# Performance work log

Measured on AMD Instinct MI355X. Metric: run time of the kernel, lower is better.

## Reference

```python
import jax, jax.numpy as jnp
import numpy as np

KERNEL_SIZE = 7  # must be odd
PAD = KERNEL_SIZE // 2


def setup_inputs() -> dict:
    key = jax.random.key(0)
    k1, k2 = jax.random.split(key)
    B, C, H, W = 8, 128, 256, 256
    x = jax.random.normal(k1, (B, C, H, W), dtype=jnp.float32)
    y = jax.random.normal(k2, (B, C, H, W), dtype=jnp.float32)
    return {"x": x, "y": y}


def reference(x, y):
    # x, y: [B, C, H, W] -> coef: [B, K*K, H, W]
    B, C, H, W = x.shape
    ypad = jnp.pad(y, ((0, 0), (0, 0), (PAD, PAD), (PAD, PAD)))  # ZeroPad2d
    coefs = []
    for i in range(KERNEL_SIZE):
        for j in range(KERNEL_SIZE):
            # shifted window of y, same spatial size as x
            yw = ypad[:, :, i:i + H, j:j + W]
            coefs.append(jnp.sum(x * yw, axis=1))  # channel dot product -> [B, H, W]
    return jnp.stack(coefs, axis=1)  # [B, K*K, H, W]
```

## Files before the change

### kernel.cpp

```cpp
#include <hip/hip_runtime.h>


#define Bq 8
#define Cq 128
#define Hq 256
#define Wq 256
#define Kq 7
#define TILE_H 8
#define TILE_W 64
#define NTHR 448
#define CS (Hq * Wq)
#define SLOT 7168
#define NSLOT 5
#define YB 4480

typedef const __attribute__((address_space(1))) void* gptr_t;
typedef __attribute__((address_space(3))) void* lptr_t;

__device__ __forceinline__ void dma16(const float* g, char* l) {
    __builtin_amdgcn_global_load_lds((gptr_t)g, (lptr_t)l, 16, 0, 0);
}

__global__ __launch_bounds__(NTHR)
__attribute__((amdgpu_waves_per_eu(4, 5)))
void corr7_kernel(const float* __restrict__ x, const float* __restrict__ y,
                  float* __restrict__ out, const float* __restrict__ zbuf)
{
    __shared__ __align__(16) char smem[NSLOT * SLOT];

    const int t    = threadIdx.x;
    const int wave = t >> 6;
    const int lane = t & 63;
    const int lw   = lane & 7;
    const int lr   = lane >> 3;

    int bid = (int)blockIdx.x;
    bid = (bid & 7) * 128 + (bid >> 3);
    const int tw = bid & 3;
    const int th = (bid >> 2) & 31;
    const int b  = bid >> 7;

    const int h0 = th * TILE_H;
    const int w0 = tw * TILE_W;
    const int wq = w0 + 8 * lw;

    const size_t base = (size_t)b * Cq * CS;

    const float* src;
    unsigned sstep;
    {
        const int k = t;
        if (k < 280) {
            const int f = 4 * k;
            const int r = f / 80, q = f - 80 * r;
            const int gy = h0 + r - 3;
            const int gx = w0 - 8 + q;
            const bool v = ((unsigned)gy < (unsigned)Hq) &&
                           ((unsigned)gx < (unsigned)Wq);
            src   = v ? (y + base + (size_t)gy * Wq + gx) : zbuf;
            sstep = v ? (unsigned)CS : 0u;
        } else if (k < 408) {
            const int f = 4 * (k - 280);
            const int r = f >> 6, q = f & 63;
            src   = x + base + (size_t)(h0 + r) * Wq + (w0 + q);
            sstep = (unsigned)CS;
        } else {
            src   = zbuf;
            sstep = 0u;
        }
    }

    const int ybase = (lr + wave) * 320 + lw * 32 + 16;
    const int xbase = YB + lr * 256 + lw * 32;

    float acc[Kq][8];
#pragma unroll
    for (int j = 0; j < Kq; ++j)
#pragma unroll
        for (int r = 0; r < 8; ++r) acc[j][r] = 0.f;

    unsigned soff_r = 0;
    unsigned soff_w = 4u * SLOT;

    dma16(src, smem + 0 * SLOT + t * 16); src += sstep;
    dma16(src, smem + 1 * SLOT + t * 16); src += sstep;
    dma16(src, smem + 2 * SLOT + t * 16); src += sstep;
    dma16(src, smem + 3 * SLOT + t * 16); src += sstep;

#define BODY(WAITSTR, DO_ISSUE)                                           \
    {                                                                     \
        asm volatile(WAITSTR ::: "memory");                               \
        __builtin_amdgcn_s_barrier();                                     \
        if (DO_ISSUE) { dma16(src, smem + soff_w + t * 16); src += sstep; } \
        const char* sr = smem + soff_r;                                   \
        const float4 q0 = *(const float4*)(sr + ybase);                   \
        const float4 q1 = *(const float4*)(sr + ybase + 16);              \
        const float4 q2 = *(const float4*)(sr + ybase + 32);              \
        const float4 q3 = *(const float4*)(sr + ybase + 48);              \
        const float4 xq0 = *(const float4*)(sr + xbase);                  \
        const float4 xq1 = *(const float4*)(sr + xbase + 16);             \
        float yf[16];                                                     \
        *(float4*)(yf)      = q0;  *(float4*)(yf + 4)  = q1;              \
        *(float4*)(yf + 8)  = q2;  *(float4*)(yf + 12) = q3;              \
        float xv[8];                                                      \
        *(float4*)(xv)      = xq0; *(float4*)(xv + 4)  = xq1;             \
        _Pragma("unroll")                                                 \
        for (int j = 0; j < Kq; ++j)                                      \
            _Pragma("unroll")                                             \
            for (int r = 0; r < 8; ++r)                                   \
                acc[j][r] = fmaf(xv[r], yf[1 + j + r], acc[j][r]);        \
        soff_w = soff_r;                                                  \
        soff_r += SLOT; if (soff_r == NSLOT * SLOT) soff_r = 0;           \
    }

#pragma unroll 1
    for (int c = 0; c < Cq - 4; ++c) {
        BODY("s_waitcnt vmcnt(3) lgkmcnt(0)", true)
    }
    BODY("s_waitcnt vmcnt(3) lgkmcnt(0)", false)
    BODY("s_waitcnt vmcnt(2) lgkmcnt(0)", false)
    BODY("s_waitcnt vmcnt(1) lgkmcnt(0)", false)
    BODY("s_waitcnt vmcnt(0) lgkmcnt(0)", false)
#undef BODY

    size_t obase = (((size_t)b * (Kq * Kq) + (size_t)wave * Kq) * Hq
                    + (h0 + lr)) * Wq + wq;
#pragma unroll
    for (int j = 0; j < Kq; ++j) {
        float4 o0 = {acc[j][0], acc[j][1], acc[j][2], acc[j][3]};
        float4 o1 = {acc[j][4], acc[j][5], acc[j][6], acc[j][7]};
        *(float4*)(out + obase)     = o0;
        *(float4*)(out + obase + 4) = o1;
        obase += (size_t)CS;
    }
}

extern "C" void kernel_launch(void* const* d_in, const int* in_sizes, int n_in,
                              void* d_out, int out_size, void* d_ws, size_t ws_size,
                              hipStream_t stream) {
    const float* x = (const float*)d_in[0];
    const float* y = (const float*)d_in[1];
    float* out = (float*)d_out;

    hipMemsetAsync(d_ws, 0, 256, stream);

    dim3 grid(Bq * 32 * 4);
    dim3 block(NTHR);
    hipLaunchKernelGGL(corr7_kernel, grid, block, 0, stream,
                       x, y, out, (const float*)d_ws);
}
```

Measured before the change: 313.2 us.

## Process two channels per barrier with six LDS slots and padded row pitches

The channel pipeline now uses six LDS slots and consumes two channels per barrier, issuing two async global-to-LDS loads per iteration, which halves the number of workgroup barriers. The LDS layout gets padded row pitches for y (336 B) and x (272 B), with extra loader threads writing zero-padding, to cut LDS bank conflicts on the float4 reads. The occupancy hint loses its upper bound. The cost is more LDS per block (six slots instead of five), which may reduce resident blocks per CU, plus more idle loader lanes for the padding columns.

```diff
diff --git a/kernel.cpp b/kernel.cpp
--- a/kernel.cpp
+++ b/kernel.cpp
@@ -11,8 +11,10 @@
 #define NTHR 448
 #define CS (Hq * Wq)
 #define SLOT 7168
-#define NSLOT 5
-#define YB 4480
+#define NSLOT 6
+#define YPITCH_B 336
+#define XBASE_B  4704
+#define XPITCH_B 272
 
 typedef const __attribute__((address_space(1))) void* gptr_t;
 typedef __attribute__((address_space(3))) void* lptr_t;
@@ -22,7 +24,7 @@
 }
 
 __global__ __launch_bounds__(NTHR)
-__attribute__((amdgpu_waves_per_eu(4, 5)))
+__attribute__((amdgpu_waves_per_eu(4)))
 void corr7_kernel(const float* __restrict__ x, const float* __restrict__ y,
                   float* __restrict__ out, const float* __restrict__ zbuf)
 {
@@ -49,29 +51,28 @@
     const float* src;
     unsigned sstep;
     {
-        const int k = t;
-        if (k < 280) {
-            const int f = 4 * k;
-            const int r = f / 80, q = f - 80 * r;
+        if (t < 294) {
+            const int r = t / 21, j = t - 21 * r;
             const int gy = h0 + r - 3;
-            const int gx = w0 - 8 + q;
-            const bool v = ((unsigned)gy < (unsigned)Hq) &&
-                           ((unsigned)gx < (unsigned)Wq);
+            const int gx = w0 - 8 + 4 * j;
+            const bool v = (j < 20) && ((unsigned)gy < (unsigned)Hq) &&
+                           (gx >= 0) && (gx + 3 < Wq);
             src   = v ? (y + base + (size_t)gy * Wq + gx) : zbuf;
             sstep = v ? (unsigned)CS : 0u;
-        } else if (k < 408) {
-            const int f = 4 * (k - 280);
-            const int r = f >> 6, q = f & 63;
-            src   = x + base + (size_t)(h0 + r) * Wq + (w0 + q);
-            sstep = (unsigned)CS;
+        } else if (t < 430) {
+            const int u = t - 294;
+            const int r = u / 17, j = u - 17 * r;
+            const bool v = (j < 16);
+            src   = v ? (x + base + (size_t)(h0 + r) * Wq + (w0 + 4 * j)) : zbuf;
+            sstep = v ? (unsigned)CS : 0u;
         } else {
             src   = zbuf;
             sstep = 0u;
         }
     }
 
-    const int ybase = (lr + wave) * 320 + lw * 32 + 16;
-    const int xbase = YB + lr * 256 + lw * 32;
+    const int yb = (lr + wave) * YPITCH_B + 32 * lw + 16;
+    const int xb = XBASE_B + lr * XPITCH_B + 32 * lw;
 
     float acc[Kq][8];
 #pragma unroll
@@ -79,49 +80,61 @@
 #pragma unroll
         for (int r = 0; r < 8; ++r) acc[j][r] = 0.f;
 
-    unsigned soff_r = 0;
-    unsigned soff_w = 4u * SLOT;
+#define COMPUTE(OFF) {                                                    \
+    const char* sr = (const char*)smem + (OFF);                           \
+    const float4 q0 = *(const float4*)(sr + yb);                          \
+    const float4 q1 = *(const float4*)(sr + yb + 16);                     \
+    const float4 q2 = *(const float4*)(sr + yb + 32);                     \
+    const float4 q3 = *(const float4*)(sr + yb + 48);                     \
+    const float4 p0 = *(const float4*)(sr + xb);                          \
+    const float4 p1 = *(const float4*)(sr + xb + 16);                     \
+    float yf[16];                                                         \
+    *(float4*)(yf)      = q0;  *(float4*)(yf + 4)  = q1;                  \
+    *(float4*)(yf + 8)  = q2;  *(float4*)(yf + 12) = q3;                  \
+    float xv[8];                                                          \
+    *(float4*)(xv)      = p0;  *(float4*)(xv + 4)  = p1;                  \
+    _Pragma("unroll")                                                     \
+    for (int j = 0; j < Kq; ++j)                                          \
+        _Pragma("unroll")                                                 \
+        for (int r = 0; r < 8; ++r)                                       \
+            acc[j][r] = fmaf(xv[r], yf[1 + j + r], acc[j][r]);            \
+}
 
-    dma16(src, smem + 0 * SLOT + t * 16); src += sstep;
-    dma16(src, smem + 1 * SLOT + t * 16); src += sstep;
-    dma16(src, smem + 2 * SLOT + t * 16); src += sstep;
-    dma16(src, smem + 3 * SLOT + t * 16); src += sstep;
-
-#define BODY(WAITSTR, DO_ISSUE)                                           \
-    {                                                                     \
-        asm volatile(WAITSTR ::: "memory");                               \
-        __builtin_amdgcn_s_barrier();                                     \
-        if (DO_ISSUE) { dma16(src, smem + soff_w + t * 16); src += sstep; } \
-        const char* sr = smem + soff_r;                                   \
-        const float4 q0 = *(const float4*)(sr + ybase);                   \
-        const float4 q1 = *(const float4*)(sr + ybase + 16);              \
-        const float4 q2 = *(const float4*)(sr + ybase + 32);              \
-        const float4 q3 = *(const float4*)(sr + ybase + 48);              \
-        const float4 xq0 = *(const float4*)(sr + xbase);                  \
-        const float4 xq1 = *(const float4*)(sr + xbase + 16);             \
-        float yf[16];                                                     \
-        *(float4*)(yf)      = q0;  *(float4*)(yf + 4)  = q1;              \
-        *(float4*)(yf + 8)  = q2;  *(float4*)(yf + 12) = q3;              \
-        float xv[8];                                                      \
-        *(float4*)(xv)      = xq0; *(float4*)(xv + 4)  = xq1;             \
-        _Pragma("unroll")                                                 \
-        for (int j = 0; j < Kq; ++j)                                      \
-            _Pragma("unroll")                                             \
-            for (int r = 0; r < 8; ++r)                                   \
-                acc[j][r] = fmaf(xv[r], yf[1 + j + r], acc[j][r]);        \
-        soff_w = soff_r;                                                  \
-        soff_r += SLOT; if (soff_r == NSLOT * SLOT) soff_r = 0;           \
+#pragma unroll
+    for (int c = 0; c < 4; ++c) {
+        dma16(src, smem + c * SLOT + t * 16);
+        src += sstep;
     }
 
+    unsigned rd = 0;
 #pragma unroll 1
-    for (int c = 0; c < Cq - 4; ++c) {
-        BODY("s_waitcnt vmcnt(3) lgkmcnt(0)", true)
+    for (int k = 0; k < 62; ++k) {
+        asm volatile("s_waitcnt vmcnt(2) lgkmcnt(0)" ::: "memory");
+        __builtin_amdgcn_s_barrier();
+        unsigned wr0 = rd + 4u * SLOT; if (wr0 >= NSLOT * SLOT) wr0 -= NSLOT * SLOT;
+        unsigned wr1 = wr0 + SLOT;     if (wr1 >= NSLOT * SLOT) wr1 -= NSLOT * SLOT;
+        dma16(src, smem + wr0 + t * 16); src += sstep;
+        dma16(src, smem + wr1 + t * 16); src += sstep;
+        COMPUTE(rd)
+        unsigned rd1 = rd + SLOT; if (rd1 >= NSLOT * SLOT) rd1 -= NSLOT * SLOT;
+        COMPUTE(rd1)
+        rd += 2u * SLOT; if (rd >= NSLOT * SLOT) rd -= NSLOT * SLOT;
     }
-    BODY("s_waitcnt vmcnt(3) lgkmcnt(0)", false)
-    BODY("s_waitcnt vmcnt(2) lgkmcnt(0)", false)
-    BODY("s_waitcnt vmcnt(1) lgkmcnt(0)", false)
-    BODY("s_waitcnt vmcnt(0) lgkmcnt(0)", false)
-#undef BODY
+    {
+        asm volatile("s_waitcnt vmcnt(2) lgkmcnt(0)" ::: "memory");
+        __builtin_amdgcn_s_barrier();
+        COMPUTE(rd)
+        unsigned rd1 = rd + SLOT; if (rd1 >= NSLOT * SLOT) rd1 -= NSLOT * SLOT;
+        COMPUTE(rd1)
+        rd += 2u * SLOT; if (rd >= NSLOT * SLOT) rd -= NSLOT * SLOT;
+
+        asm volatile("s_waitcnt vmcnt(0) lgkmcnt(0)" ::: "memory");
+        __builtin_amdgcn_s_barrier();
+        COMPUTE(rd)
+        rd1 = rd + SLOT; if (rd1 >= NSLOT * SLOT) rd1 -= NSLOT * SLOT;
+        COMPUTE(rd1)
+    }
+#undef COMPUTE
 
     size_t obase = (((size_t)b * (Kq * Kq) + (size_t)wave * Kq) * Hq
                     + (h0 + lr)) * Wq + wq;
```

Result: no change. 309.4 us (-1.2%).
